# Kernel optimization log

Hardware: AMD Instinct MI355X
Metric: run time of the kernel (lower is better)

## Reference

```python
import jax, jax.numpy as jnp
import numpy as np
import math

B, H, S, D = 2, 16, 2048, 64

def setup_inputs() -> dict:
    key = jax.random.key(0)
    kq, kk, kv = jax.random.split(key, 3)
    Q = jax.random.normal(kq, (B, H, S, D), dtype=jnp.float32)
    K = jax.random.normal(kk, (B, H, S, D), dtype=jnp.float32)
    V = jax.random.normal(kv, (B, H, S, D), dtype=jnp.float32)
    causal_mask = jnp.tril(jnp.ones((S, S), dtype=bool))
    return {"Q": Q, "K": K, "V": V, "causal_mask": causal_mask}

def reference(Q, K, V, causal_mask):
    d_k = K.shape[-1]
    scores = jnp.einsum('bhqd,bhkd->bhqk', Q, K) / math.sqrt(d_k)
    scores = jnp.where(causal_mask, scores, -jnp.inf)
    probs = jax.nn.softmax(scores, axis=-1)
    return jnp.einsum('bhqk,bhkd->bhqd', probs, V)
```

## Files before the change

### kernel.cpp

```cpp
#include <hip/hip_runtime.h>
#include <math.h>


constexpr int kS   = 2048;
constexpr int kD   = 64;
constexpr int kBH  = 32;
constexpr int kPadP = 72;

typedef short short8 __attribute__((ext_vector_type(8)));
typedef float float4v __attribute__((ext_vector_type(4)));
typedef float float16v __attribute__((ext_vector_type(16)));
typedef unsigned int u32;
typedef unsigned short u16;

static __device__ inline u16 f2bf(float f) {
  union { float f; unsigned u; } v; v.f = f;
  unsigned r = v.u + 0x7FFF + ((v.u >> 16) & 1);
  return (u16)(r >> 16);
}

static __device__ inline short8 pack8(float4v a, float4v b) {
  short8 r;
  r[0] = (short)f2bf(a[0]); r[1] = (short)f2bf(a[1]);
  r[2] = (short)f2bf(a[2]); r[3] = (short)f2bf(a[3]);
  r[4] = (short)f2bf(b[0]); r[5] = (short)f2bf(b[1]);
  r[6] = (short)f2bf(b[2]); r[7] = (short)f2bf(b[3]);
  return r;
}

static __device__ inline void async_cp16(const void* g, void* l) {
  __builtin_amdgcn_global_load_lds(
      (const __attribute__((address_space(1))) u32*)g,
      (__attribute__((address_space(3))) u32*)l, 16, 0, 0);
}

__global__ __launch_bounds__(256)
void prep_kernel(const float* __restrict__ Q, const float* __restrict__ K,
                 const float* __restrict__ V,
                 u16* __restrict__ Qb, u16* __restrict__ Kb, u16* __restrict__ VT) {
  __shared__ u16 tile[64 * kPadP];
  const int tid = threadIdx.x;
  const int bh = blockIdx.y, st = blockIdx.x;
  const size_t ibase = (size_t)bh * kS * kD + (size_t)st * 64 * kD;
  const int r  = tid >> 2;
  const int c0 = (tid & 3) * 16;
  {
    const float scl = 0.125f * 1.44269504089f;
    const float* qp = Q + ibase + (size_t)r * kD + c0;
    float4v a = *(const float4v*)(qp);
    float4v b = *(const float4v*)(qp + 4);
    float4v c = *(const float4v*)(qp + 8);
    float4v d = *(const float4v*)(qp + 12);
    #pragma unroll
    for (int i = 0; i < 4; ++i) { a[i] *= scl; b[i] *= scl; c[i] *= scl; d[i] *= scl; }
    u16* dst = Qb + ibase + (size_t)r * kD + c0;
    *(short8*)dst       = pack8(a, b);
    *(short8*)(dst + 8) = pack8(c, d);
  }
  {
    const float* kp = K + ibase + (size_t)r * kD + c0;
    float4v a = *(const float4v*)(kp);
    float4v b = *(const float4v*)(kp + 4);
    float4v c = *(const float4v*)(kp + 8);
    float4v d = *(const float4v*)(kp + 12);
    u16* dst = Kb + ibase + (size_t)r * kD + c0;
    *(short8*)dst       = pack8(a, b);
    *(short8*)(dst + 8) = pack8(c, d);
  }
  {
    const float* vp = V + ibase + (size_t)r * kD + c0;
    float4v a = *(const float4v*)(vp);
    float4v b = *(const float4v*)(vp + 4);
    float4v c = *(const float4v*)(vp + 8);
    float4v d = *(const float4v*)(vp + 12);
    u16* t = &tile[r * kPadP + c0];
    *(short8*)t       = pack8(a, b);
    *(short8*)(t + 8) = pack8(c, d);
  }
  __syncthreads();
  {
    const int dd = tid >> 2;
    const int s0 = (tid & 3) * 16;
    short8 w0, w1;
    #pragma unroll
    for (int i = 0; i < 8; ++i) {
      w0[i] = (short)tile[(s0 + i) * kPadP + dd];
      w1[i] = (short)tile[(s0 + 8 + i) * kPadP + dd];
    }
    u16* vdst = VT + (size_t)bh * kD * kS + (size_t)dd * kS + st * 64 + s0;
    *(short8*)vdst       = w0;
    *(short8*)(vdst + 8) = w1;
  }
}

__global__ __launch_bounds__(256, 2)
void fattn_kernel(const u16* __restrict__ Qb, const u16* __restrict__ Kb,
                  const u16* __restrict__ VT,
                  u32* __restrict__ O0, u32* __restrict__ O1,
                  u32* __restrict__ O2, u32* __restrict__ O3,
                  float* __restrict__ Lp) {
  __shared__ __align__(16) u16 ldsK[2][4096];
  __shared__ __align__(16) u16 ldsV[2][4096];

  const int tid  = threadIdx.x;
  const int wave = tid >> 6;
  const int lane = tid & 63;
  const int l31  = lane & 31;
  const int h    = lane >> 5;

  const int bh = blockIdx.y;
  const int p  = blockIdx.x >> 2;
  const int z  = blockIdx.x & 3;
  const int qiA = p, qiB = 7 - p;
  const int nA  = 4 * p + 4;

  const size_t base  = (size_t)bh * kS * kD;
  const size_t vbase = (size_t)bh * kD * kS;

  const int lr  = lane >> 3;
  const int cxl = (lane & 7) ^ lr;
  const int offK0 = lr * 64   + cxl * 8;
  const int offV0 = lr * 2048 + cxl * 8;
  const unsigned hs16 = ((unsigned)(h ^ (l31 & 7))) * 16;

  u32* Od = (z == 0) ? O0 : (z == 1) ? O1 : (z == 2) ? O2 : O3;
  const int cB = 9 * z;
  const int cE = cB + 9;

  short8 ones;
  #pragma unroll
  for (int i = 0; i < 8; ++i) ones[i] = (short)0x3F80;

  int par = 0;
  for (int seg = 0; seg < 2; ++seg) {
    const int qi = seg ? qiB : qiA;
    int tb, te;
    if (seg == 0) { tb = min(cB, nA); te = min(cE, nA); }
    else          { tb = max(cB, nA) - nA; te = max(cE, nA) - nA; }
    const int wq0 = qi * 256 + wave * 64;

    short8 qf[2][4];
    #pragma unroll
    for (int g = 0; g < 2; ++g) {
      const u16* qp = Qb + base + (size_t)(wq0 + 32 * g + l31) * kD + h * 8;
      #pragma unroll
      for (int dk = 0; dk < 4; ++dk) qf[g][dk] = *(const short8*)(qp + dk * 16);
    }

    float16v acc[2][2], lacc[2];
    #pragma unroll
    for (int g = 0; g < 2; ++g) {
      #pragma unroll
      for (int i = 0; i < 16; ++i) { acc[g][0][i] = 0.f; acc[g][1][i] = 0.f; lacc[g][i] = 0.f; }
    }

    if (tb < te) {
      {
        const u16* kg0 = Kb + base + (size_t)tb * 4096;
        const u16* vg0 = VT + vbase + tb * 64;
        const int b = par & 1;
        #pragma unroll
        for (int j = 0; j < 2; ++j) {
          const int g = wave + 4 * j;
          async_cp16(kg0 + g * 512 + offK0,           &ldsK[b][g * 512]);
          async_cp16(vg0 + (size_t)g * 16384 + offV0, &ldsV[b][g * 512]);
        }
      }
      for (int t = tb; t < te; ++t, ++par) {
        __syncthreads();
        if (t + 1 < te) {
          const u16* kg0 = Kb + base + (size_t)(t + 1) * 4096;
          const u16* vg0 = VT + vbase + (t + 1) * 64;
          const int b = (par + 1) & 1;
          #pragma unroll
          for (int j = 0; j < 2; ++j) {
            const int g = wave + 4 * j;
            async_cp16(kg0 + g * 512 + offK0,           &ldsK[b][g * 512]);
            async_cp16(vg0 + (size_t)g * 16384 + offV0, &ldsV[b][g * 512]);
          }
        }
        const char* KB = (const char*)ldsK[par & 1];
        const char* VB = (const char*)ldsV[par & 1];
        #pragma unroll
        for (int kt32 = 0; kt32 < 2; ++kt32) {
          const int ktb = t * 64 + kt32 * 32;
          if (ktb > wq0 + 63) break;

          const char* krow = KB + (kt32 * 32 + l31) * 128;
          short8 kf[4];
          #pragma unroll
          for (int dk = 0; dk < 4; ++dk)
            kf[dk] = *(const short8*)(krow + (((unsigned)(dk * 32)) ^ hs16));
          short8 vf[4];
          #pragma unroll
          for (int c = 0; c < 2; ++c) {
            const unsigned coff = ((unsigned)((kt32 * 4 + 2 * c) * 16)) ^ hs16;
            vf[2 * c]     = *(const short8*)(VB + l31 * 128 + coff);
            vf[2 * c + 1] = *(const short8*)(VB + (32 + l31) * 128 + coff);
          }

          #pragma unroll
          for (int g = 0; g < 2; ++g) {
            if (ktb > wq0 + 32 * g + 31) continue;

            float16v s;
            #pragma unroll
            for (int i = 0; i < 16; ++i) s[i] = 0.f;
            #pragma unroll
            for (int dk = 0; dk < 4; ++dk)
              s = __builtin_amdgcn_mfma_f32_32x32x16_bf16(kf[dk], qf[g][dk], s, 0, 0, 0);

            if (ktb == wq0 + 32 * g) {
              const int qg = wq0 + 32 * g + l31;
              #pragma unroll
              for (int r = 0; r < 16; ++r) {
                const int kg = ktb + (r & 3) + 8 * (r >> 2) + 4 * h;
                if (kg > qg) s[r] = -1e30f;
              }
            }

            u32 pk[8];
            #pragma unroll
            for (int g2 = 0; g2 < 4; ++g2) {
              const u32 u0 = __float_as_uint(__builtin_amdgcn_exp2f(s[4 * g2 + 0]));
              const u32 u1 = __float_as_uint(__builtin_amdgcn_exp2f(s[4 * g2 + 1]));
              const u32 u2 = __float_as_uint(__builtin_amdgcn_exp2f(s[4 * g2 + 2]));
              const u32 u3 = __float_as_uint(__builtin_amdgcn_exp2f(s[4 * g2 + 3]));
              pk[2 * g2]     = __builtin_amdgcn_perm(u1, u0, 0x07060302u);
              pk[2 * g2 + 1] = __builtin_amdgcn_perm(u3, u2, 0x07060302u);
            }
            u32 ek[8];
            #pragma unroll
            for (int i = 0; i < 8; ++i) ek[i] = (u32)__shfl_xor((int)pk[i], 32);

            #pragma unroll
            for (int c = 0; c < 2; ++c) {
              const int ga = 4 * c, gb = 4 * c + 2;
              union { u32 u[4]; short8 s8; } pf;
              pf.u[0] = h ? ek[gb]     : pk[ga];
              pf.u[1] = h ? ek[gb + 1] : pk[ga + 1];
              pf.u[2] = h ? pk[gb]     : ek[ga];
              pf.u[3] = h ? pk[gb + 1] : ek[ga + 1];
              acc[g][0] = __builtin_amdgcn_mfma_f32_32x32x16_bf16(pf.s8, vf[2 * c],     acc[g][0], 0, 0, 0);
              acc[g][1] = __builtin_amdgcn_mfma_f32_32x32x16_bf16(pf.s8, vf[2 * c + 1], acc[g][1], 0, 0, 0);
              lacc[g]   = __builtin_amdgcn_mfma_f32_32x32x16_bf16(pf.s8, ones,          lacc[g],   0, 0, 0);
            }
          }
        }
      }
    }

    #pragma unroll
    for (int g = 0; g < 2; ++g) {
      #pragma unroll
      for (int r = 0; r < 16; ++r) {
        const int row = (r & 3) + 8 * (r >> 2) + 4 * h;
        const u32 w = (u32)f2bf(acc[g][0][r]) | ((u32)f2bf(acc[g][1][r]) << 16);
        Od[((size_t)bh * kS + wq0 + 32 * g + row) * 32 + l31] = w;
      }
      if (l31 == 0) {
        #pragma unroll
        for (int r = 0; r < 16; ++r) {
          const int row = (r & 3) + 8 * (r >> 2) + 4 * h;
          Lp[(size_t)z * kBH * kS + (size_t)bh * kS + wq0 + 32 * g + row] = lacc[g][r];
        }
      }
    }
  }
}

__global__ __launch_bounds__(256)
void combine_kernel(const u32* __restrict__ O0, const u32* __restrict__ O1,
                    const u32* __restrict__ O2, const u32* __restrict__ O3,
                    const float* __restrict__ Lp, float* __restrict__ O) {
  const int idx = blockIdx.x * 256 + threadIdx.x;
  const int row = idx >> 5;
  const int j   = idx & 31;
  const int N = kBH * kS;
  const float l = Lp[row] + Lp[N + row] + Lp[2 * N + row] + Lp[3 * N + row];
  const float inv = 1.f / l;
  const u32 a = O0[idx], b = O1[idx], c = O2[idx], d = O3[idx];
  const float lo = __uint_as_float(a << 16) + __uint_as_float(b << 16)
                 + __uint_as_float(c << 16) + __uint_as_float(d << 16);
  const float hi = __uint_as_float(a & 0xFFFF0000u) + __uint_as_float(b & 0xFFFF0000u)
                 + __uint_as_float(c & 0xFFFF0000u) + __uint_as_float(d & 0xFFFF0000u);
  float* op = O + (size_t)row * kD;
  op[j]      = lo * inv;
  op[j + 32] = hi * inv;
}

extern "C" void kernel_launch(void* const* d_in, const int* in_sizes, int n_in,
                              void* d_out, int out_size, void* d_ws, size_t ws_size,
                              hipStream_t stream) {
  const float* Q = (const float*)d_in[0];
  const float* K = (const float*)d_in[1];
  const float* V = (const float*)d_in[2];
  float* O = (float*)d_out;

  const size_t nKV = (size_t)kBH * kS * kD;
  u16* Qb = (u16*)d_ws;
  u16* Kb = Qb + nKV;
  u16* VT = Kb + nKV;
  u32* O0 = (u32*)(VT + nKV);
  u32* O1 = O0 + nKV / 2;
  u32* O2 = O1 + nKV / 2;
  u32* O3 = O2 + nKV / 2;
  float* Lp = (float*)(O3 + nKV / 2);

  dim3 gprep(kS / 64, kBH);
  prep_kernel<<<gprep, 256, 0, stream>>>(Q, K, V, Qb, Kb, VT);
  dim3 grid(16, kBH);
  fattn_kernel<<<grid, 256, 0, stream>>>(Qb, Kb, VT, O0, O1, O2, O3, Lp);
  combine_kernel<<<(int)(kBH * kS * 32 / 256), 256, 0, stream>>>(O0, O1, O2, O3, Lp, O);
}
```

Before: 144.9 us.

## Use permlane32_swap for half-wave exchange and issue both QK MFMA chains upfront

Replaces the per-register shfl_xor (ds_bpermute) plus selects used to rearrange exp'd probabilities with a permlane32_swap builtin when available, cutting LDS-path cross-lane traffic. It also hoists both query-group score MFMA chains ahead of the softmax/PV loop so the two independent chains can interleave and hide MFMA latency. The cost is higher register pressure from keeping two score accumulators live, which may affect occupancy.

Measured after the change: 146.0 us. About the same (+0.8%).

```diff
diff --git a/kernel.cpp b/kernel.cpp
--- a/kernel.cpp
+++ b/kernel.cpp
@@ -32,6 +32,20 @@
   __builtin_amdgcn_global_load_lds(
       (const __attribute__((address_space(1))) u32*)g,
       (__attribute__((address_space(3))) u32*)l, 16, 0, 0);
+}
+
+static __device__ inline void xhalf(u32 pga, u32 pgb, u32& lo, u32& hi) {
+#if __has_builtin(__builtin_amdgcn_permlane32_swap)
+  auto r = __builtin_amdgcn_permlane32_swap(pga, pgb, false, false);
+  lo = r[0];
+  hi = r[1];
+#else
+  const u32 ea = (u32)__shfl_xor((int)pga, 32);
+  const u32 eb = (u32)__shfl_xor((int)pgb, 32);
+  const bool top = (threadIdx.x & 32) != 0;
+  lo = top ? eb : pga;
+  hi = top ? pgb : ea;
+#endif
 }
 
 __global__ __launch_bounds__(256)
@@ -185,6 +199,7 @@
         for (int kt32 = 0; kt32 < 2; ++kt32) {
           const int ktb = t * 64 + kt32 * 32;
           if (ktb > wq0 + 63) break;
+          const bool live0 = (ktb <= wq0 + 31);
 
           const char* krow = KB + (kt32 * 32 + l31) * 128;
           short8 kf[4];
@@ -199,16 +214,22 @@
             vf[2 * c + 1] = *(const short8*)(VB + (32 + l31) * 128 + coff);
           }
 
-          #pragma unroll
-          for (int g = 0; g < 2; ++g) {
-            if (ktb > wq0 + 32 * g + 31) continue;
-
-            float16v s;
-            #pragma unroll
-            for (int i = 0; i < 16; ++i) s[i] = 0.f;
+          float16v s0, s1;
+          #pragma unroll
+          for (int i = 0; i < 16; ++i) { s0[i] = 0.f; s1[i] = 0.f; }
+          if (live0) {
             #pragma unroll
             for (int dk = 0; dk < 4; ++dk)
-              s = __builtin_amdgcn_mfma_f32_32x32x16_bf16(kf[dk], qf[g][dk], s, 0, 0, 0);
+              s0 = __builtin_amdgcn_mfma_f32_32x32x16_bf16(kf[dk], qf[0][dk], s0, 0, 0, 0);
+          }
+          #pragma unroll
+          for (int dk = 0; dk < 4; ++dk)
+            s1 = __builtin_amdgcn_mfma_f32_32x32x16_bf16(kf[dk], qf[1][dk], s1, 0, 0, 0);
+
+          #pragma unroll
+          for (int g = 0; g < 2; ++g) {
+            if (g == 0 && !live0) continue;
+            float16v& s = g ? s1 : s0;
 
             if (ktb == wq0 + 32 * g) {
               const int qg = wq0 + 32 * g + l31;
@@ -229,18 +250,13 @@
               pk[2 * g2]     = __builtin_amdgcn_perm(u1, u0, 0x07060302u);
               pk[2 * g2 + 1] = __builtin_amdgcn_perm(u3, u2, 0x07060302u);
             }
-            u32 ek[8];
-            #pragma unroll
-            for (int i = 0; i < 8; ++i) ek[i] = (u32)__shfl_xor((int)pk[i], 32);
 
             #pragma unroll
             for (int c = 0; c < 2; ++c) {
               const int ga = 4 * c, gb = 4 * c + 2;
               union { u32 u[4]; short8 s8; } pf;
-              pf.u[0] = h ? ek[gb]     : pk[ga];
-              pf.u[1] = h ? ek[gb + 1] : pk[ga + 1];
-              pf.u[2] = h ? pk[gb]     : ek[ga];
-              pf.u[3] = h ? pk[gb + 1] : ek[ga + 1];
+              xhalf(pk[ga],     pk[gb],     pf.u[0], pf.u[2]);
+              xhalf(pk[ga + 1], pk[gb + 1], pf.u[1], pf.u[3]);
               acc[g][0] = __builtin_amdgcn_mfma_f32_32x32x16_bf16(pf.s8, vf[2 * c],     acc[g][0], 0, 0, 0);
               acc[g][1] = __builtin_amdgcn_mfma_f32_32x32x16_bf16(pf.s8, vf[2 * c + 1], acc[g][1], 0, 0, 0);
               lacc[g]   = __builtin_amdgcn_mfma_f32_32x32x16_bf16(pf.s8, ones,          lacc[g],   0, 0, 0);
```
